# Kernel tuning notes

Hardware: AMD Instinct MI355X
Metric: run time of the kernel (lower is better)

## Reference

```python
import jax, jax.numpy as jnp
import numpy as np

BN_EPS = 1e-5
N_NODES = 50000


def _bn(h, g, b, m, v):
    # BatchNorm1d in inference mode: running stats
    return (h - m) * (g / jnp.sqrt(v + BN_EPS)) + b


def _gin_agg(x, src, dst):
    # GINConv with eps=0: (1+eps)*x + sum_{j in N(i)} x_j
    agg = jax.ops.segment_sum(x[src], dst, num_segments=x.shape[0])
    return x + agg


def setup_inputs() -> dict:
    key = jax.random.key(0)
    ks = jax.random.split(key, 24)
    N, E, C_in, H, C_out = N_NODES, 800000, 128, 128, 64
    x = jax.random.normal(ks[0], (N, C_in), dtype=jnp.float32)
    edge_index = jax.random.randint(ks[1], (2, E), 0, N, dtype=jnp.int64)

    def lin(k, i, o):
        s = 1.0 / np.sqrt(i)
        return jax.random.uniform(k, (i, o), jnp.float32, -s, s)

    def bnp(k, d):
        k1, k2 = jax.random.split(k)
        return (jnp.ones((d,), jnp.float32), jnp.zeros((d,), jnp.float32),
                jax.random.normal(k1, (d,), jnp.float32) * 0.1,
                jax.random.uniform(k2, (d,), jnp.float32, 0.5, 1.5))
    g0, be0, m0, v0 = bnp(ks[4], H)
    g1, be1, m1, v1 = bnp(ks[5], H)
    g2, be2, m2, v2 = bnp(ks[6], H)
    return {
        "x": x, "edge_index": edge_index,
        "W0": lin(ks[7], C_in, H), "b0": jnp.zeros((H,), jnp.float32),
        "g0": g0, "be0": be0, "m0": m0, "v0": v0,
        "W1": lin(ks[8], H, H), "b1": jnp.zeros((H,), jnp.float32),
        "g1": g1, "be1": be1, "m1": m1, "v1": v1,
        "W2": lin(ks[9], H, H), "b2": jnp.zeros((H,), jnp.float32),
        "g2": g2, "be2": be2, "m2": m2, "v2": v2,
        "W3": lin(ks[10], H, C_out), "b3": jnp.zeros((C_out,), jnp.float32),
    }


def reference(x, edge_index, W0, b0, g0, be0, m0, v0,
              W1, b1, g1, be1, m1, v1,
              W2, b2, g2, be2, m2, v2, W3, b3):
    src, dst = edge_index[0], edge_index[1]
    # layer 0: GINConv(firstmlp) -> relu (dropout identity in eval)
    h = _gin_agg(x, src, dst)
    h = jax.nn.relu(_bn(h @ W0 + b0, g0, be0, m0, v0))  # firstmlp
    h = jax.nn.relu(h)
    # layer 1: GINConv(mlp) -> relu
    h = _gin_agg(h, src, dst)
    h = jax.nn.relu(_bn(h @ W1 + b1, g1, be1, m1, v1))  # mlp
    h = jax.nn.relu(h)
    # layer 2: GINConv(lastmlp); if_auc=True -> raw output
    h = _gin_agg(h, src, dst)
    h = jax.nn.relu(_bn(h @ W2 + b2, g2, be2, m2, v2))
    out = h @ W3 + b3
    return out
```

## Files before the change

### kernel.cpp

```cpp
#include <hip/hip_runtime.h>

#define HDIM 128
#define NBMAX 512
#define CAPB 2560

typedef __attribute__((ext_vector_type(8))) short short8;
typedef __attribute__((ext_vector_type(4))) float f32x4;

__device__ __forceinline__ short f2bf(float f) {
    union { float f; unsigned u; } x; x.f = f;
    unsigned r = x.u + 0x7FFF + ((x.u >> 16) & 1);
    return (short)(r >> 16);
}
__device__ __forceinline__ float bf2f(short s) {
    union { unsigned u; float f; } x;
    x.u = ((unsigned)(unsigned short)s) << 16;
    return x.f;
}

__global__ void cvt_bf16(short* __restrict__ dst, const float* __restrict__ src, int n) {
    int i = (blockIdx.x * blockDim.x + threadIdx.x) * 4;
    int stride = gridDim.x * blockDim.x * 4;
    for (; i < n; i += stride) {
        float4 v = *(const float4*)(src + i);
        short4 o;
        o.x = f2bf(v.x); o.y = f2bf(v.y); o.z = f2bf(v.z); o.w = f2bf(v.w);
        *(short4*)(dst + i) = o;
    }
}

__global__ __launch_bounds__(256) void scatter_recs(int* __restrict__ recs, int* __restrict__ bucketCur,
                                                    const int* __restrict__ srci, const int* __restrict__ dsti,
                                                    int E, int NB) {
    __shared__ int hist[NBMAX];
    __shared__ int gb[NBMAX];
    const int t = threadIdx.x;
    const int base = blockIdx.x * 4096;
    for (int b = t; b < NBMAX; b += 256) hist[b] = 0;
    __syncthreads();
    #pragma unroll
    for (int i = 0; i < 16; i++) {
        int e = base + i * 256 + t;
        if (e < E) atomicAdd(&hist[dsti[e] >> 7], 1);
    }
    __syncthreads();
    for (int b = t; b < NB; b += 256) {
        int c = hist[b];
        gb[b] = c ? atomicAdd(&bucketCur[b], c) : 0;
        hist[b] = 0;
    }
    __syncthreads();
    #pragma unroll
    for (int i = 0; i < 16; i++) {
        int e = base + i * 256 + t;
        if (e < E) {
            int d = dsti[e], s = srci[e];
            int b = d >> 7;
            int off = atomicAdd(&hist[b], 1);
            int pos = gb[b] + off;
            if (pos < CAPB) recs[b * CAPB + pos] = ((d & 127) << 16) | s;
        }
    }
}

__global__ __launch_bounds__(256) void build_csr_local(
        unsigned short* __restrict__ csrH, int* __restrict__ rowdesc,
        const int* __restrict__ recs, const int* __restrict__ bucketCur, int N) {
    const int b = blockIdx.x;
    const int base = b * CAPB;
    int cnt = bucketCur[b]; if (cnt > CAPB) cnt = CAPB;
    __shared__ int nh[128];
    __shared__ int cur[128];
    const int t = threadIdx.x;
    if (t < 128) nh[t] = 0;
    __syncthreads();
    for (int i = t; i < cnt; i += 256) atomicAdd(&nh[recs[base + i] >> 16], 1);
    __syncthreads();
    if (t < 64) {
        int lane = t;
        int c0 = nh[lane], c1 = nh[64 + lane];
        int i0 = c0;
        #pragma unroll
        for (int s = 1; s < 64; s <<= 1) { int n = __shfl_up(i0, s, 64); if (lane >= s) i0 += n; }
        int tot0 = __shfl(i0, 63, 64);
        int i1 = c1;
        #pragma unroll
        for (int s = 1; s < 64; s <<= 1) { int n = __shfl_up(i1, s, 64); if (lane >= s) i1 += n; }
        i1 += tot0;
        int e0 = i0 - c0, e1 = i1 - c1;
        cur[lane] = e0; cur[64 + lane] = e1;
        int idx0 = b * 128 + lane, idx1 = b * 128 + 64 + lane;
        int d0 = c0 > 127 ? 127 : c0, d1 = c1 > 127 ? 127 : c1;
        if (idx0 < N) rowdesc[idx0] = ((base + e0) << 7) | d0;
        if (idx1 < N) rowdesc[idx1] = ((base + e1) << 7) | d1;
    }
    __syncthreads();
    for (int i = t; i < cnt; i += 256) {
        int r = recs[base + i];
        int off = atomicAdd(&cur[r >> 16], 1);
        csrH[base + off] = (unsigned short)(r & 0xffff);
    }
}

__global__ void prep_all(short* __restrict__ Wp0, short* __restrict__ Wp1,
                         short* __restrict__ Wp2, short* __restrict__ Wp3,
                         const float* __restrict__ W0, const float* __restrict__ W1,
                         const float* __restrict__ W2, const float* __restrict__ W3,
                         float* __restrict__ scbuf, int* __restrict__ bucketCur,
                         const float* __restrict__ b0, const float* __restrict__ g0,
                         const float* __restrict__ be0, const float* __restrict__ m0,
                         const float* __restrict__ v0,
                         const float* __restrict__ b1, const float* __restrict__ g1,
                         const float* __restrict__ be1, const float* __restrict__ m1,
                         const float* __restrict__ v1,
                         const float* __restrict__ b2, const float* __restrict__ g2,
                         const float* __restrict__ be2, const float* __restrict__ m2,
                         const float* __restrict__ v2,
                         const float* __restrict__ b3) {
    int bid = blockIdx.x;
    if (bid < 24) {
        int layer = bid >> 3;
        int tid = (bid & 7) * 256 + threadIdx.x;
        const float* W = layer == 0 ? W0 : layer == 1 ? W1 : W2;
        short* Wp = layer == 0 ? Wp0 : layer == 1 ? Wp1 : Wp2;
        int lane = tid & 63;
        int ks = (tid >> 6) & 3;
        int nt = tid >> 8;
        int n = nt * 16 + (lane & 15);
        int k0 = ks * 32 + ((lane >> 4) & 3) * 8;
        short8 v;
        #pragma unroll
        for (int j = 0; j < 8; j++) v[j] = f2bf(W[(long)(k0 + j) * HDIM + n]);
        ((short8*)Wp)[tid] = v;
    } else if (bid < 28) {
        int tid = (bid - 24) * 256 + threadIdx.x;
        int lane = tid & 63;
        int ks = (tid >> 6) & 3;
        int nt = tid >> 8;
        int n = nt * 16 + (lane & 15);
        int k0 = ks * 32 + ((lane >> 4) & 3) * 8;
        short8 v;
        #pragma unroll
        for (int j = 0; j < 8; j++) v[j] = f2bf(W3[(long)(k0 + j) * 64 + n]);
        ((short8*)Wp3)[tid] = v;
    } else if (bid == 28) {
        for (int iter = 0; iter < 2; iter++) {
            int slot = iter * 256 + threadIdx.x;
            if (slot < 128) {
                int c = slot;
                float s = g0[c] * rsqrtf(v0[c] + 1e-5f);
                scbuf[c] = s;
                scbuf[128 + c] = (b0[c] - m0[c]) * s + be0[c];
            } else if (slot < 256) {
                int c = slot - 128;
                float s = g1[c] * rsqrtf(v1[c] + 1e-5f);
                scbuf[256 + c] = s;
                scbuf[256 + 128 + c] = (b1[c] - m1[c]) * s + be1[c];
            } else if (slot < 384) {
                int c = slot - 256;
                float s = g2[c] * rsqrtf(v2[c] + 1e-5f);
                scbuf[512 + c] = s;
                scbuf[512 + 128 + c] = (b2[c] - m2[c]) * s + be2[c];
            } else if (slot < 448) {
                int c = slot - 384;
                scbuf[768 + c] = 1.f;
                scbuf[768 + 128 + c] = b3[c];
            }
        }
    } else {
        bucketCur[threadIdx.x] = 0;
        bucketCur[256 + threadIdx.x] = 0;
    }
}

template<bool FINAL>
__global__ __launch_bounds__(256) void gin_layer(
        short* __restrict__ outb, float* __restrict__ outf,
        const short* __restrict__ xp,
        const int* __restrict__ rowdesc, const unsigned short* __restrict__ csrH,
        const short* __restrict__ Wp,
        const float* __restrict__ scale, const float* __restrict__ offset,
        const short* __restrict__ Wp2,
        const float* __restrict__ scale2, const float* __restrict__ offset2,
        int N) {
    __shared__ short As[16 * HDIM];
    const int t = threadIdx.x;
    const int row0 = blockIdx.x * 16;

    {
        const short8* xp8 = (const short8*)xp;
        int rl = t >> 4;
        int chunk = t & 15;
        int node = row0 + rl;
        float facc[8];
        if (node < N) {
            short8 id = xp8[(long)node * 16 + chunk];
            #pragma unroll
            for (int j = 0; j < 8; j++) facc[j] = bf2f(id[j]);
            int v = rowdesc[node];
            int deg = v & 127;
            const unsigned short* nb = csrH + (v >> 7);
            int k = 0;
            for (; k + 4 <= deg; k += 4) {
                int n0 = nb[k], n1 = nb[k + 1], n2 = nb[k + 2], n3 = nb[k + 3];
                short8 v0 = xp8[(long)n0 * 16 + chunk];
                short8 v1 = xp8[(long)n1 * 16 + chunk];
                short8 v2 = xp8[(long)n2 * 16 + chunk];
                short8 v3 = xp8[(long)n3 * 16 + chunk];
                #pragma unroll
                for (int j = 0; j < 8; j++)
                    facc[j] += (bf2f(v0[j]) + bf2f(v1[j])) + (bf2f(v2[j]) + bf2f(v3[j]));
            }
            for (; k < deg; k++) {
                short8 v0 = xp8[(long)nb[k] * 16 + chunk];
                #pragma unroll
                for (int j = 0; j < 8; j++) facc[j] += bf2f(v0[j]);
            }
        } else {
            #pragma unroll
            for (int j = 0; j < 8; j++) facc[j] = 0.f;
        }
        short8 o;
        #pragma unroll
        for (int j = 0; j < 8; j++) o[j] = f2bf(facc[j]);
        int baddr = (rl * 256 + chunk * 16) ^ ((rl & 7) << 4);
        *(short8*)((char*)As + baddr) = o;
    }
    __syncthreads();

    const int lane = t & 63, w = t >> 6;
    const int rl0 = lane & 15;
    const int hi = (lane >> 4) & 3;
    short8 a[4];
    #pragma unroll
    for (int ks = 0; ks < 4; ks++) {
        int baddr = (rl0 * 256 + ks * 64 + hi * 16) ^ ((rl0 & 7) << 4);
        a[ks] = *(const short8*)((const char*)As + baddr);
    }
    if (FINAL) __syncthreads();

    const short8* bp = (const short8*)Wp + lane;
    const int c = lane & 15;
    const int rb = hi * 4;

    #pragma unroll
    for (int i = 0; i < 2; i++) {
        int nt = w * 2 + i;
        f32x4 acc = {0.f, 0.f, 0.f, 0.f};
        short8 b0 = bp[(nt * 4 + 0) * 64];
        short8 b1 = bp[(nt * 4 + 1) * 64];
        short8 b2 = bp[(nt * 4 + 2) * 64];
        short8 b3 = bp[(nt * 4 + 3) * 64];
        acc = __builtin_amdgcn_mfma_f32_16x16x32_bf16(a[0], b0, acc, 0, 0, 0);
        acc = __builtin_amdgcn_mfma_f32_16x16x32_bf16(a[1], b1, acc, 0, 0, 0);
        acc = __builtin_amdgcn_mfma_f32_16x16x32_bf16(a[2], b2, acc, 0, 0, 0);
        acc = __builtin_amdgcn_mfma_f32_16x16x32_bf16(a[3], b3, acc, 0, 0, 0);
        int cc = nt * 16 + c;
        float s = scale[cc], o = offset[cc];
        if (!FINAL) {
            #pragma unroll
            for (int r = 0; r < 4; r++) {
                int rr = row0 + rb + r;
                if (rr < N) {
                    float val = fmaxf(acc[r] * s + o, 0.f);
                    outb[(long)rr * HDIM + cc] = f2bf(val);
                }
            }
        } else {
            #pragma unroll
            for (int r = 0; r < 4; r++) {
                int rloc = rb + r;
                float val = fmaxf(acc[r] * s + o, 0.f);
                int baddr = (rloc * 256 + cc * 2) ^ ((rloc & 7) << 4);
                *(short*)((char*)As + baddr) = f2bf(val);
            }
        }
    }

    if (FINAL) {
        __syncthreads();
        short8 a2[4];
        #pragma unroll
        for (int ks = 0; ks < 4; ks++) {
            int baddr = (rl0 * 256 + ks * 64 + hi * 16) ^ ((rl0 & 7) << 4);
            a2[ks] = *(const short8*)((const char*)As + baddr);
        }
        const short8* bp2 = (const short8*)Wp2 + lane;
        int nt = w;
        f32x4 acc = {0.f, 0.f, 0.f, 0.f};
        short8 b0 = bp2[(nt * 4 + 0) * 64];
        short8 b1 = bp2[(nt * 4 + 1) * 64];
        short8 b2 = bp2[(nt * 4 + 2) * 64];
        short8 b3v = bp2[(nt * 4 + 3) * 64];
        acc = __builtin_amdgcn_mfma_f32_16x16x32_bf16(a2[0], b0, acc, 0, 0, 0);
        acc = __builtin_amdgcn_mfma_f32_16x16x32_bf16(a2[1], b1, acc, 0, 0, 0);
        acc = __builtin_amdgcn_mfma_f32_16x16x32_bf16(a2[2], b2, acc, 0, 0, 0);
        acc = __builtin_amdgcn_mfma_f32_16x16x32_bf16(a2[3], b3v, acc, 0, 0, 0);
        int cc = nt * 16 + c;
        float s2 = scale2[cc], o2 = offset2[cc];
        #pragma unroll
        for (int r = 0; r < 4; r++) {
            int rr = row0 + rb + r;
            if (rr < N) outf[(long)rr * 64 + cc] = acc[r] * s2 + o2;
        }
    }
}

extern "C" void kernel_launch(void* const* d_in, const int* in_sizes, int n_in,
                              void* d_out, int out_size, void* d_ws, size_t ws_size,
                              hipStream_t stream) {
    const float* x  = (const float*)d_in[0];
    const int*   ei = (const int*)d_in[1];
    const int E = in_sizes[1] / 2;
    const int* srci = ei;
    const int* dsti = ei + E;

    const float* W0 = (const float*)d_in[2];
    const float* b0 = (const float*)d_in[3];
    const float* g0 = (const float*)d_in[4];
    const float* be0 = (const float*)d_in[5];
    const float* m0 = (const float*)d_in[6];
    const float* v0 = (const float*)d_in[7];
    const float* W1 = (const float*)d_in[8];
    const float* b1 = (const float*)d_in[9];
    const float* g1 = (const float*)d_in[10];
    const float* be1 = (const float*)d_in[11];
    const float* m1 = (const float*)d_in[12];
    const float* v1 = (const float*)d_in[13];
    const float* W2 = (const float*)d_in[14];
    const float* b2 = (const float*)d_in[15];
    const float* g2 = (const float*)d_in[16];
    const float* be2 = (const float*)d_in[17];
    const float* m2 = (const float*)d_in[18];
    const float* v2 = (const float*)d_in[19];
    const float* W3 = (const float*)d_in[20];
    const float* b3 = (const float*)d_in[21];

    const int N = in_sizes[0] / HDIM;
    const int NB = (N + 127) >> 7;
    float* out = (float*)d_out;

    short* ba = (short*)d_ws;
    short* bb = ba + (size_t)N * HDIM;
    int* rowdesc = (int*)(bb + (size_t)N * HDIM);
    int* recs   = rowdesc + ((N + 3) & ~3);
    unsigned short* csrH = (unsigned short*)(recs + (size_t)NB * CAPB);
    int* bucketCur = (int*)(((uintptr_t)(csrH + (size_t)NB * CAPB) + 63) & ~(uintptr_t)63);
    short* Wp0 = (short*)(((uintptr_t)(bucketCur + NBMAX) + 63) & ~(uintptr_t)63);
    short* Wp1  = Wp0 + 16384;
    short* Wp2  = Wp1 + 16384;
    short* Wp3  = Wp2 + 16384;
    float* scbuf = (float*)(Wp3 + 8192);

    const int layerBlocks = (N + 15) / 16;
    const int nElem = N * HDIM;
    int cvtBlocks = (nElem / 4 + 255) / 256; if (cvtBlocks > 2048) cvtBlocks = 2048;

    prep_all<<<30, 256, 0, stream>>>(Wp0, Wp1, Wp2, Wp3, W0, W1, W2, W3, scbuf, bucketCur,
                                     b0, g0, be0, m0, v0,
                                     b1, g1, be1, m1, v1,
                                     b2, g2, be2, m2, v2, b3);
    cvt_bf16<<<cvtBlocks, 256, 0, stream>>>(ba, x, nElem);
    scatter_recs<<<(E + 4095) / 4096, 256, 0, stream>>>(recs, bucketCur, srci, dsti, E, NB);
    build_csr_local<<<NB, 256, 0, stream>>>(csrH, rowdesc, recs, bucketCur, N);

    gin_layer<false><<<layerBlocks, 256, 0, stream>>>(
        bb, nullptr, ba, rowdesc, csrH, Wp0, scbuf + 0, scbuf + 128,
        nullptr, nullptr, nullptr, N);
    gin_layer<false><<<layerBlocks, 256, 0, stream>>>(
        ba, nullptr, bb, rowdesc, csrH, Wp1, scbuf + 256, scbuf + 384,
        nullptr, nullptr, nullptr, N);
    gin_layer<true><<<layerBlocks, 256, 0, stream>>>(
        nullptr, out, ba, rowdesc, csrH, Wp2, scbuf + 512, scbuf + 640,
        Wp3, scbuf + 768, scbuf + 896, N);
}
```

Baseline: 148.5 us.

## Sort nodes by degree within buckets to balance gather work per wavefront

The CSR build now also computes, for each 128-node bucket, a permutation that orders nodes by in-degree via a counting sort in shared memory. The GIN layer kernels process nodes in this permuted order and scatter results back through the permutation. The aim is that the 16 rows handled by each block have similar degrees, which reduces divergence and idle lanes in the neighbor-gather loop. In exchange it adds an indirection load per row, non-contiguous output writes, and some extra shared-memory work in the build kernel. The old build_csr_local is left behind in a broken state, but it is never launched.

Measured after the change: 165.4 us. +11.3%, slower.

```diff
diff --git a/kernel.cpp b/kernel.cpp
--- a/kernel.cpp
+++ b/kernel.cpp
@@ -64,15 +64,17 @@
 }
 
 __global__ __launch_bounds__(256) void build_csr_local(
-        unsigned short* __restrict__ csrH, int* __restrict__ rowdesc,
+        unsigned short* __restrict__ csrH, int* __restrict__ rowdesc, int* __restrict__ perm,
         const int* __restrict__ recs, const int* __restrict__ bucketCur, int N) {
     const int b = blockIdx.x;
     const int base = b * CAPB;
     int cnt = bucketCur[b]; if (cnt > CAPB) cnt = CAPB;
+    const int valid = min(128, N - b * 128);
     __shared__ int nh[128];
     __shared__ int cur[128];
+    __shared__ int degBase[128];
     const int t = threadIdx.x;
-    if (t < 128) nh[t] = 0;
+    if (t < 128) { nh[t] = 0; degBase[t] = 0; }
     __syncthreads();
     for (int i = t; i < cnt; i += 256) atomicAdd(&nh[recs[base + i] >> 16], 1);
     __syncthreads();
@@ -94,11 +96,35 @@
         if (idx0 < N) rowdesc[idx0] = ((base + e0) << 7) | d0;
         if (idx1 < N) rowdesc[idx1] = ((base + e1) << 7) | d1;
     }
+    if (t < valid) { int d = nh[t] > 127 ? 127 : nh[t]; atomicAdd(&degBase[d], 1); }
+    __syncthreads();
+    if (t < 64) {
+        int lane = t;
+        int c0 = degBase[lane], c1 = degBase[64 + lane];
+        int i0 = c0;
+        #pragma unroll
+        for (int s = 1; s < 64; s <<= 1) { int n = __shfl_up(i0, s, 64); if (lane >= s) i0 += n; }
+        int tot0 = __shfl(i0, 63, 64);
+        int i1 = c1;
+        #pragma unroll
+        for (int s = 1; s < 64; s <<= 1) { int n = __shfl_up(i1, s, 64); if (lane >= s) i1 += n; }
+        i1 += tot0;
+        cur[lane] = i0 - c0; cur[64 + lane] = i1 - c1;
+    }
+    __syncthreads();
+    if (false) {}
+    if (t < valid) {
+        int d = nh[t] > 127 ? 127 : nh[t];
+        int pos = atomicAdd(&cur[d], 1);
+        perm[b * 128 + pos] = b * 128 + t;
+    }
     __syncthreads();
     for (int i = t; i < cnt; i += 256) {
         int r = recs[base + i];
-        int off = atomicAdd(&cur[r >> 16], 1);
-        csrH[base + off] = (unsigned short)(r & 0xffff);
+        int ln = r >> 16;
+        int start = (rowdesc[b * 128 + ln] >> 7);
+        int off = atomicAdd(&nh[ln], 1) - nh[ln];
+        (void)start; (void)off;
     }
 }
 
@@ -178,12 +204,14 @@
         short* __restrict__ outb, float* __restrict__ outf,
         const short* __restrict__ xp,
         const int* __restrict__ rowdesc, const unsigned short* __restrict__ csrH,
+        const int* __restrict__ perm,
         const short* __restrict__ Wp,
         const float* __restrict__ scale, const float* __restrict__ offset,
         const short* __restrict__ Wp2,
         const float* __restrict__ scale2, const float* __restrict__ offset2,
         int N) {
     __shared__ short As[16 * HDIM];
+    __shared__ int pr[16];
     const int t = threadIdx.x;
     const int row0 = blockIdx.x * 16;
 
@@ -191,9 +219,11 @@
         const short8* xp8 = (const short8*)xp;
         int rl = t >> 4;
         int chunk = t & 15;
-        int node = row0 + rl;
+        int slot = row0 + rl;
         float facc[8];
-        if (node < N) {
+        if (slot < N) {
+            int node = perm[slot];
+            if (chunk == 0) pr[rl] = node;
             short8 id = xp8[(long)node * 16 + chunk];
             #pragma unroll
             for (int j = 0; j < 8; j++) facc[j] = bf2f(id[j]);
@@ -260,10 +290,10 @@
         if (!FINAL) {
             #pragma unroll
             for (int r = 0; r < 4; r++) {
-                int rr = row0 + rb + r;
-                if (rr < N) {
+                int slot = row0 + rb + r;
+                if (slot < N) {
                     float val = fmaxf(acc[r] * s + o, 0.f);
-                    outb[(long)rr * HDIM + cc] = f2bf(val);
+                    outb[(long)pr[rb + r] * HDIM + cc] = f2bf(val);
                 }
             }
         } else {
@@ -300,9 +330,71 @@
         float s2 = scale2[cc], o2 = offset2[cc];
         #pragma unroll
         for (int r = 0; r < 4; r++) {
-            int rr = row0 + rb + r;
-            if (rr < N) outf[(long)rr * 64 + cc] = acc[r] * s2 + o2;
-        }
+            int slot = row0 + rb + r;
+            if (slot < N) outf[(long)pr[rb + r] * 64 + cc] = acc[r] * s2 + o2;
+        }
+    }
+}
+
+__global__ __launch_bounds__(256) void build_csr_sort(
+        unsigned short* __restrict__ csrH, int* __restrict__ rowdesc, int* __restrict__ perm,
+        const int* __restrict__ recs, const int* __restrict__ bucketCur, int N) {
+    const int b = blockIdx.x;
+    const int base = b * CAPB;
+    int cnt = bucketCur[b]; if (cnt > CAPB) cnt = CAPB;
+    const int valid = min(128, N - b * 128);
+    __shared__ int nh[128];
+    __shared__ int cur[128];
+    __shared__ int degh[128];
+    const int t = threadIdx.x;
+    if (t < 128) { nh[t] = 0; degh[t] = 0; }
+    __syncthreads();
+    for (int i = t; i < cnt; i += 256) atomicAdd(&nh[recs[base + i] >> 16], 1);
+    __syncthreads();
+    if (t < 64) {
+        int lane = t;
+        int c0 = nh[lane], c1 = nh[64 + lane];
+        int i0 = c0;
+        #pragma unroll
+        for (int s = 1; s < 64; s <<= 1) { int n = __shfl_up(i0, s, 64); if (lane >= s) i0 += n; }
+        int tot0 = __shfl(i0, 63, 64);
+        int i1 = c1;
+        #pragma unroll
+        for (int s = 1; s < 64; s <<= 1) { int n = __shfl_up(i1, s, 64); if (lane >= s) i1 += n; }
+        i1 += tot0;
+        int e0 = i0 - c0, e1 = i1 - c1;
+        cur[lane] = e0; cur[64 + lane] = e1;
+        int idx0 = b * 128 + lane, idx1 = b * 128 + 64 + lane;
+        int d0 = c0 > 127 ? 127 : c0, d1 = c1 > 127 ? 127 : c1;
+        if (idx0 < N) rowdesc[idx0] = ((base + e0) << 7) | d0;
+        if (idx1 < N) rowdesc[idx1] = ((base + e1) << 7) | d1;
+    }
+    if (t < valid) { int d = nh[t] > 127 ? 127 : nh[t]; atomicAdd(&degh[d], 1); }
+    __syncthreads();
+    for (int i = t; i < cnt; i += 256) {
+        int r = recs[base + i];
+        int off = atomicAdd(&cur[r >> 16], 1);
+        csrH[base + off] = (unsigned short)(r & 0xffff);
+    }
+    __syncthreads();
+    if (t < 64) {
+        int lane = t;
+        int c0 = degh[lane], c1 = degh[64 + lane];
+        int i0 = c0;
+        #pragma unroll
+        for (int s = 1; s < 64; s <<= 1) { int n = __shfl_up(i0, s, 64); if (lane >= s) i0 += n; }
+        int tot0 = __shfl(i0, 63, 64);
+        int i1 = c1;
+        #pragma unroll
+        for (int s = 1; s < 64; s <<= 1) { int n = __shfl_up(i1, s, 64); if (lane >= s) i1 += n; }
+        i1 += tot0;
+        cur[lane] = i0 - c0; cur[64 + lane] = i1 - c1;
+    }
+    __syncthreads();
+    if (t < valid) {
+        int d = nh[t] > 127 ? 127 : nh[t];
+        int pos = atomicAdd(&cur[d], 1);
+        perm[b * 128 + pos] = b * 128 + t;
     }
 }
 
@@ -343,7 +435,8 @@
     short* ba = (short*)d_ws;
     short* bb = ba + (size_t)N * HDIM;
     int* rowdesc = (int*)(bb + (size_t)N * HDIM);
-    int* recs   = rowdesc + ((N + 3) & ~3);
+    int* perm    = rowdesc + ((N + 3) & ~3);
+    int* recs    = perm + ((N + 3) & ~3);
     unsigned short* csrH = (unsigned short*)(recs + (size_t)NB * CAPB);
     int* bucketCur = (int*)(((uintptr_t)(csrH + (size_t)NB * CAPB) + 63) & ~(uintptr_t)63);
     short* Wp0 = (short*)(((uintptr_t)(bucketCur + NBMAX) + 63) & ~(uintptr_t)63);
@@ -362,15 +455,15 @@
                                      b2, g2, be2, m2, v2, b3);
     cvt_bf16<<<cvtBlocks, 256, 0, stream>>>(ba, x, nElem);
     scatter_recs<<<(E + 4095) / 4096, 256, 0, stream>>>(recs, bucketCur, srci, dsti, E, NB);
-    build_csr_local<<<NB, 256, 0, stream>>>(csrH, rowdesc, recs, bucketCur, N);
+    build_csr_sort<<<NB, 256, 0, stream>>>(csrH, rowdesc, perm, recs, bucketCur, N);
 
     gin_layer<false><<<layerBlocks, 256, 0, stream>>>(
-        bb, nullptr, ba, rowdesc, csrH, Wp0, scbuf + 0, scbuf + 128,
+        bb, nullptr, ba, rowdesc, csrH, perm, Wp0, scbuf + 0, scbuf + 128,
         nullptr, nullptr, nullptr, N);
     gin_layer<false><<<layerBlocks, 256, 0, stream>>>(
-        ba, nullptr, bb, rowdesc, csrH, Wp1, scbuf + 256, scbuf + 384,
+        ba, nullptr, bb, rowdesc, csrH, perm, Wp1, scbuf + 256, scbuf + 384,
         nullptr, nullptr, nullptr, N);
     gin_layer<true><<<layerBlocks, 256, 0, stream>>>(
-        nullptr, out, ba, rowdesc, csrH, Wp2, scbuf + 512, scbuf + 640,
+        nullptr, out, ba, rowdesc, csrH, perm, Wp2, scbuf + 512, scbuf + 640,
         Wp3, scbuf + 768, scbuf + 896, N);
 }
```
